# Kernel tuning notes

Hardware: AMD Instinct MI355X
Metric: run time of the kernel (lower is better)

The kernel has to match this reference:

```python
import jax, jax.numpy as jnp
import numpy as np

B, S, L = 512, 512, 128


def setup_inputs() -> dict:
    key = jax.random.key(0)
    k1, k2, k3, k4 = jax.random.split(key, 4)
    return {
        "input": jax.random.normal(k1, (B, S, L), dtype=jnp.float32),
        "label": jax.random.randint(k2, (B, S), 0, L),
        "length": jax.random.randint(k3, (B,), 1, S + 1),
        "trans": jax.random.uniform(k4, (L, L), dtype=jnp.float32),
    }


def reference(input, label, length, trans):
    b, s, l = input.shape
    length = jnp.clip(length, 1, s)
    # sequence mask [B, S]
    mask = (jnp.arange(s)[None, :] < length[:, None]).astype(input.dtype)
    x = input * mask[:, :, None]  # masked emissions, as in call()

    # --- gold path score (compute_path_score, via gathers instead of dense one-hot outer products) ---
    point_score = jnp.sum(
        jnp.take_along_axis(x, label[:, :, None], axis=2)[:, :, 0] * mask,
        axis=1, keepdims=True)
    pair_mask = mask[:, :-1] * mask[:, 1:]
    trans_score = jnp.sum(trans[label[:, :-1], label[:, 1:]] * pair_mask,
                          axis=1, keepdims=True)
    label_score = point_score + trans_score  # [B, 1]

    # --- forward algorithm (comput_z recurrence) as lax.scan ---
    def step(alpha, xt):
        # alpha: [B, L] prev forward vars; xt: [B, L] emissions at t
        alpha = jax.nn.logsumexp(alpha[:, :, None] + trans[None, :, :], axis=1) + xt
        return alpha, alpha

    alpha0 = x[:, 0, :]
    xs = jnp.swapaxes(x, 0, 1)[1:]  # [S-1, B, L]
    _, alphas = jax.lax.scan(step, alpha0, xs)
    alphas = jnp.concatenate([alpha0[None], alphas], axis=0)  # [S, B, L]

    # pick forward vars at the last valid position of each sequence
    final_scores = alphas[length - 1, jnp.arange(b)]  # [B, L]
    z = jax.nn.logsumexp(final_scores, axis=1, keepdims=True)  # [B, 1]
    return z - label_score
```

## Files before the change

### kernel.cpp

```cpp
#include <hip/hip_runtime.h>

#define BB 512
#define SS 512
#define LL 128

__global__ void __launch_bounds__(256) crf_label_score_kernel(
    const float* __restrict__ input, const int* __restrict__ label,
    const int* __restrict__ length, const float* __restrict__ trans,
    float* __restrict__ ls)
{
    const int b = blockIdx.x;
    const int tid = threadIdx.x;
    int len = length[b];
    len = len < 1 ? 1 : (len > SS ? SS : len);

    float acc = 0.f;
    for (int t = tid; t < len; t += 256) {
        const int lab = label[b * SS + t];
        acc += input[((size_t)b * SS + t) * LL + lab];
        if (t + 1 < len) {
            const int lab2 = label[b * SS + t + 1];
            acc += trans[lab * LL + lab2];
        }
    }
    #pragma unroll
    for (int off = 32; off > 0; off >>= 1) acc += __shfl_xor(acc, off, 64);
    __shared__ float wpart[4];
    if ((tid & 63) == 0) wpart[tid >> 6] = acc;
    __syncthreads();
    if (tid == 0) ls[b] = wpart[0] + wpart[1] + wpart[2] + wpart[3];
}

__global__ void __launch_bounds__(128) crf_forward_kernel(
    const float* __restrict__ input, const int* __restrict__ length,
    const float* __restrict__ trans, const float* __restrict__ ls,
    float* __restrict__ out)
{
    const int b = blockIdx.x;
    const int j = threadIdx.x;
    int len = length[b];
    len = len < 1 ? 1 : (len > SS ? SS : len);

    __shared__ float e_lds[LL];
    __shared__ float wred[2];
    __shared__ float wsum[2];

    float tcol[LL];
    #pragma unroll
    for (int i = 0; i < LL; ++i)
        tcol[i] = __expf(trans[i * LL + j]);

    const float* __restrict__ xb = input + (size_t)b * SS * LL;
    float alpha = xb[j];

    for (int t = 1; t < len; ++t) {
        const float xt = xb[t * LL + j];

        float m = alpha;
        #pragma unroll
        for (int off = 32; off > 0; off >>= 1) m = fmaxf(m, __shfl_xor(m, off, 64));
        if ((j & 63) == 0) wred[j >> 6] = m;
        __syncthreads();
        const float M = fmaxf(wred[0], wred[1]);

        e_lds[j] = __expf(alpha - M);
        __syncthreads();

        float acc0 = 0.f, acc1 = 0.f, acc2 = 0.f, acc3 = 0.f;
        const float4* __restrict__ e4 = reinterpret_cast<const float4*>(e_lds);
        #pragma unroll
        for (int i = 0; i < LL / 4; ++i) {
            const float4 ev = e4[i];
            acc0 = fmaf(ev.x, tcol[4 * i + 0], acc0);
            acc1 = fmaf(ev.y, tcol[4 * i + 1], acc1);
            acc2 = fmaf(ev.z, tcol[4 * i + 2], acc2);
            acc3 = fmaf(ev.w, tcol[4 * i + 3], acc3);
        }
        alpha = M + __logf((acc0 + acc1) + (acc2 + acc3)) + xt;
    }

    float m = alpha;
    #pragma unroll
    for (int off = 32; off > 0; off >>= 1) m = fmaxf(m, __shfl_xor(m, off, 64));
    if ((j & 63) == 0) wred[j >> 6] = m;
    __syncthreads();
    const float M = fmaxf(wred[0], wred[1]);

    float ex = __expf(alpha - M);
    #pragma unroll
    for (int off = 32; off > 0; off >>= 1) ex += __shfl_xor(ex, off, 64);
    if ((j & 63) == 0) wsum[j >> 6] = ex;
    __syncthreads();

    if (j == 0) out[b] = M + __logf(wsum[0] + wsum[1]) - ls[b];
}

extern "C" void kernel_launch(void* const* d_in, const int* in_sizes, int n_in,
                              void* d_out, int out_size, void* d_ws, size_t ws_size,
                              hipStream_t stream) {
    const float* input  = (const float*)d_in[0];
    const int*   label  = (const int*)d_in[1];
    const int*   length = (const int*)d_in[2];
    const float* trans  = (const float*)d_in[3];
    float* out = (float*)d_out;
    float* ls  = (float*)d_ws;

    crf_label_score_kernel<<<BB, 256, 0, stream>>>(input, label, length, trans, ls);
    crf_forward_kernel<<<BB, 128, 0, stream>>>(input, length, trans, ls, out);
}
```

Measured before the change: 683.4 us.

## Split forward recurrence across thread pairs, double-buffer LDS, and prefetch emissions

The forward kernel now uses 256 threads with two threads per label, each summing half of the transition column, and combines the halves with a shuffle. The LDS exp buffer and the max-reduction slots are double-buffered, so each timestep needs only one barrier. The running max is taken from the previous step's alpha rather than recomputed before the exp. Emissions are prefetched three steps ahead to hide global latency on the serial chain. The tradeoff is halved per-thread register arrays but more threads per block, an extra shuffle per step, and a stale max that could lose numerical safety if alpha grows by a large amount in a single step.

```diff
diff --git a/kernel.cpp b/kernel.cpp
--- a/kernel.cpp
+++ b/kernel.cpp
@@ -31,68 +31,101 @@
     if (tid == 0) ls[b] = wpart[0] + wpart[1] + wpart[2] + wpart[3];
 }
 
-__global__ void __launch_bounds__(128) crf_forward_kernel(
+__global__ void __launch_bounds__(256) crf_forward_kernel(
     const float* __restrict__ input, const int* __restrict__ length,
     const float* __restrict__ trans, const float* __restrict__ ls,
     float* __restrict__ out)
 {
-    const int b = blockIdx.x;
-    const int j = threadIdx.x;
+    const int b    = blockIdx.x;
+    const int tid  = threadIdx.x;
+    const int j    = tid >> 1;
+    const int h    = tid & 1;
+    const int w    = tid >> 6;
+    const int lane = tid & 63;
+
     int len = length[b];
     len = len < 1 ? 1 : (len > SS ? SS : len);
 
-    __shared__ float e_lds[LL];
-    __shared__ float wred[2];
-    __shared__ float wsum[2];
+    __shared__ float e_lds[2][LL];
+    __shared__ float wmax[2][4];
+    __shared__ float wpre[4];
+    __shared__ float wfin[8];
 
-    float tcol[LL];
+    float tcol[64];
     #pragma unroll
-    for (int i = 0; i < LL; ++i)
-        tcol[i] = __expf(trans[i * LL + j]);
+    for (int k = 0; k < 64; ++k)
+        tcol[k] = __expf(trans[(h * 64 + k) * LL + j]);
 
     const float* __restrict__ xb = input + (size_t)b * SS * LL;
     float alpha = xb[j];
 
-    for (int t = 1; t < len; ++t) {
-        const float xt = xb[t * LL + j];
-
+    {
         float m = alpha;
         #pragma unroll
-        for (int off = 32; off > 0; off >>= 1) m = fmaxf(m, __shfl_xor(m, off, 64));
-        if ((j & 63) == 0) wred[j >> 6] = m;
-        __syncthreads();
-        const float M = fmaxf(wred[0], wred[1]);
+        for (int off = 2; off <= 32; off <<= 1) m = fmaxf(m, __shfl_xor(m, off, 64));
+        if (lane == 0) wpre[w] = m;
+    }
+    __syncthreads();
+    float M_cur = fmaxf(fmaxf(wpre[0], wpre[1]), fmaxf(wpre[2], wpre[3]));
 
-        e_lds[j] = __expf(alpha - M);
+    float x_a = (1 < len) ? xb[1 * LL + j] : 0.f;
+    float x_b = (2 < len) ? xb[2 * LL + j] : 0.f;
+    float x_c = (3 < len) ? xb[3 * LL + j] : 0.f;
+
+    for (int t = 1; t < len; ++t) {
+        const int buf = t & 1;
+        const float xt = x_a;
+        x_a = x_b; x_b = x_c;
+        const int tf = t + 3;
+        x_c = (tf < len) ? xb[tf * LL + j] : 0.f;
+
+        const float e = __expf(alpha - M_cur);
+        if (h == 0) e_lds[buf][j] = e;
+
+        float mm = alpha;
+        #pragma unroll
+        for (int off = 2; off <= 32; off <<= 1) mm = fmaxf(mm, __shfl_xor(mm, off, 64));
+        if (lane == 0) wmax[buf][w] = mm;
+
         __syncthreads();
 
         float acc0 = 0.f, acc1 = 0.f, acc2 = 0.f, acc3 = 0.f;
-        const float4* __restrict__ e4 = reinterpret_cast<const float4*>(e_lds);
+        const float4* __restrict__ e4 =
+            reinterpret_cast<const float4*>(&e_lds[buf][h * 64]);
         #pragma unroll
-        for (int i = 0; i < LL / 4; ++i) {
-            const float4 ev = e4[i];
-            acc0 = fmaf(ev.x, tcol[4 * i + 0], acc0);
-            acc1 = fmaf(ev.y, tcol[4 * i + 1], acc1);
-            acc2 = fmaf(ev.z, tcol[4 * i + 2], acc2);
-            acc3 = fmaf(ev.w, tcol[4 * i + 3], acc3);
+        for (int k = 0; k < 16; ++k) {
+            const float4 ev = e4[k];
+            acc0 = fmaf(ev.x, tcol[4 * k + 0], acc0);
+            acc1 = fmaf(ev.y, tcol[4 * k + 1], acc1);
+            acc2 = fmaf(ev.z, tcol[4 * k + 2], acc2);
+            acc3 = fmaf(ev.w, tcol[4 * k + 3], acc3);
         }
-        alpha = M + __logf((acc0 + acc1) + (acc2 + acc3)) + xt;
+        float s = (acc0 + acc1) + (acc2 + acc3);
+        s += __shfl_xor(s, 1, 64);
+
+        alpha = M_cur + __logf(s) + xt;
+
+        M_cur = fmaxf(fmaxf(wmax[buf][0], wmax[buf][1]),
+                      fmaxf(wmax[buf][2], wmax[buf][3]));
     }
 
-    float m = alpha;
+    {
+        float mf = alpha;
+        #pragma unroll
+        for (int off = 2; off <= 32; off <<= 1) mf = fmaxf(mf, __shfl_xor(mf, off, 64));
+        if (lane == 0) wfin[w] = mf;
+    }
+    __syncthreads();
+    const float M = fmaxf(fmaxf(wfin[0], wfin[1]), fmaxf(wfin[2], wfin[3]));
+
+    float ex = (h == 0) ? __expf(alpha - M) : 0.f;
     #pragma unroll
-    for (int off = 32; off > 0; off >>= 1) m = fmaxf(m, __shfl_xor(m, off, 64));
-    if ((j & 63) == 0) wred[j >> 6] = m;
-    __syncthreads();
-    const float M = fmaxf(wred[0], wred[1]);
-
-    float ex = __expf(alpha - M);
-    #pragma unroll
-    for (int off = 32; off > 0; off >>= 1) ex += __shfl_xor(ex, off, 64);
-    if ((j & 63) == 0) wsum[j >> 6] = ex;
+    for (int off = 1; off <= 32; off <<= 1) ex += __shfl_xor(ex, off, 64);
+    if (lane == 0) wfin[4 + w] = ex;
     __syncthreads();
 
-    if (j == 0) out[b] = M + __logf(wsum[0] + wsum[1]) - ls[b];
+    if (tid == 0)
+        out[b] = M + __logf(wfin[4] + wfin[5] + wfin[6] + wfin[7]) - ls[b];
 }
 
 extern "C" void kernel_launch(void* const* d_in, const int* in_sizes, int n_in,
@@ -106,5 +139,5 @@
     float* ls  = (float*)d_ws;
 
     crf_label_score_kernel<<<BB, 256, 0, stream>>>(input, label, length, trans, ls);
-    crf_forward_kernel<<<BB, 128, 0, stream>>>(input, length, trans, ls, out);
+    crf_forward_kernel<<<BB, 256, 0, stream>>>(input, length, trans, ls, out);
 }
```

After: 561.3 us. -17.9%, faster.
